# Kernel tuning notes

Measured on AMD Instinct MI355X. Metric: run time of the kernel, lower is better.

The kernel has to match this reference:

```python
import jax, jax.numpy as jnp
import numpy as np

B, S, D, H = 2, 4096, 1024, 16
HD = D // H  # 64


def setup_inputs() -> dict:
    key = jax.random.key(0)
    ks = jax.random.split(key, 6)
    return {
        "x": jax.random.normal(ks[0], (B, S, D), dtype=jnp.float32),
        "mask": jax.random.normal(ks[1], (B, S, S), dtype=jnp.float32),
        "Wqkv": jax.random.normal(ks[2], (D, 3 * D), dtype=jnp.float32) * 0.02,
        "bqkv": jax.random.normal(ks[3], (3 * D,), dtype=jnp.float32) * 0.02,
        "Wo": jax.random.normal(ks[4], (D, D), dtype=jnp.float32) * 0.02,
        "bo": jax.random.normal(ks[5], (D,), dtype=jnp.float32) * 0.02,
    }


def reference(x, mask, Wqkv, bqkv, Wo, bo):
    b, s, d = x.shape
    # fused QKV projection: [B,S,3D]
    qkv = jnp.einsum('bsd,de->bse', x, Wqkv) + bqkv
    # [B,S,H,3*HD] -> [B,H,S,3*HD]
    qkv = qkv.reshape(b, s, H, 3 * HD).transpose(0, 2, 1, 3)
    q, k, v = jnp.split(qkv, 3, axis=-1)  # each [B,H,S,HD]
    scale = 1.0 / jnp.sqrt(jnp.asarray(HD, dtype=x.dtype))
    scores = jnp.einsum('bhqe,bhke->bhqk', q, k) * scale  # [B,H,S,S]
    scores = scores + mask[:, None, :, :]  # additive mask broadcast over heads
    attn = jax.nn.softmax(scores, axis=-1)
    values = jnp.einsum('bhqk,bhke->bhqe', attn, v)  # [B,H,S,HD]
    # NOTE: faithful to original TF code: reshape WITHOUT transposing heads back
    values = values.reshape(b, s, d)
    out = jnp.einsum('bsd,de->bse', values, Wo) + bo
    return out
```

## Files before the change

kernel.cpp:

```cpp
#include <hip/hip_runtime.h>
#include <hip/hip_bf16.h>

#define DEV __device__ __forceinline__

typedef unsigned short u16;
typedef __attribute__((ext_vector_type(4))) float f32x4;
typedef __attribute__((ext_vector_type(8))) short s16x8;

static constexpr int Bc = 2, Hc = 16, Sc = 4096, Dc = 1024, HDc = 64;

DEV u16 f2bf(float f) {
  unsigned x = __float_as_uint(f);
  x += 0x7FFFu + ((x >> 16) & 1u);
  return (u16)(x >> 16);
}
DEV u16 f2bf_rn(float f) {
  return (u16)((__float_as_uint(f) + 0x8000u) >> 16);
}
DEV float bf2f(u16 u) { return __uint_as_float(((unsigned)u) << 16); }

DEV void gload_lds16(const void* g, void* l) {
  __builtin_amdgcn_global_load_lds((const __attribute__((address_space(1))) void*)g,
                                   (__attribute__((address_space(3))) void*)l, 16, 0, 0);
}

DEV f32x4 mfma16(s16x8 a, s16x8 b, f32x4 c) {
  return __builtin_amdgcn_mfma_f32_16x16x32_bf16(a, b, c, 0, 0, 0);
}

DEV f32x4 fzero4() { f32x4 v; v[0] = v[1] = v[2] = v[3] = 0.f; return v; }

__global__ void cvt_f32_bf16(const float* __restrict__ in, u16* __restrict__ out, size_t n,
                             float scale) {
  size_t i = ((size_t)blockIdx.x * blockDim.x + threadIdx.x) * 4;
  size_t stride = (size_t)gridDim.x * blockDim.x * 4;
  for (; i < n; i += stride) {
    float4 v = *(const float4*)(in + i);
    u16 a = f2bf(v.x * scale), b = f2bf(v.y * scale), c = f2bf(v.z * scale), d = f2bf(v.w * scale);
    *(ushort4*)(out + i) = make_ushort4(a, b, c, d);
  }
}

__global__ void transpose_cvt(const float* __restrict__ in, u16* __restrict__ out, int R, int C) {
  __shared__ u16 t[64][72];
  int nct = C >> 6;
  int tr = blockIdx.x / nct, tc = blockIdx.x % nct;
  int r0 = tr << 6, c0 = tc << 6;
  int lr = threadIdx.x >> 2;
  int lc0 = (threadIdx.x & 3) << 4;
  const float* src = in + (size_t)(r0 + lr) * C + c0 + lc0;
#pragma unroll
  for (int j = 0; j < 16; j += 4) {
    float4 v = *(const float4*)(src + j);
    t[lr][lc0 + j + 0] = f2bf(v.x);
    t[lr][lc0 + j + 1] = f2bf(v.y);
    t[lr][lc0 + j + 2] = f2bf(v.z);
    t[lr][lc0 + j + 3] = f2bf(v.w);
  }
  __syncthreads();
  u16* dst = out + (size_t)(c0 + lr) * R + r0 + lc0;
#pragma unroll
  for (int j = 0; j < 16; j += 4) {
    u16 a = t[lc0 + j + 0][lr], b = t[lc0 + j + 1][lr], c = t[lc0 + j + 2][lr], d = t[lc0 + j + 3][lr];
    *(ushort4*)(dst + j) = make_ushort4(a, b, c, d);
  }
}

template <int MODE>
__global__ __launch_bounds__(256, 2) void gemm128(
    const u16* __restrict__ A, const u16* __restrict__ BT, const float* __restrict__ bias,
    void* __restrict__ out0, u16* __restrict__ out1, u16* __restrict__ out2,
    int N, int K, int grid_n) {
  __shared__ u16 Al[128 * 64];
  __shared__ u16 Bl[128 * 64];
  int bid = blockIdx.x;
  int bn = bid % grid_n, bm = bid / grid_n;
  int m0 = bm * 128, n0 = bn * 128;
  int tid = threadIdx.x, lane = tid & 63, wid = tid >> 6;
  int wm = wid >> 1, wn = wid & 1;
  int fr = lane & 15, fg = lane >> 4;

  f32x4 acc[4][4];
#pragma unroll
  for (int mi = 0; mi < 4; ++mi)
#pragma unroll
    for (int ni = 0; ni < 4; ++ni) acc[mi][ni] = fzero4();

  for (int kt = 0; kt < K; kt += 64) {
    const u16* Ag = A + (size_t)m0 * K + kt;
    const u16* Bg = BT + (size_t)n0 * K + kt;
#pragma unroll
    for (int it = 0; it < 4; ++it) {
      int L = it * 4096 + wid * 1024 + lane * 16;
      int row = L >> 7;
      int sch = ((L >> 4) & 7) ^ (row & 7);
      gload_lds16(Ag + (size_t)row * K + sch * 8, (char*)Al + it * 4096 + wid * 1024);
      gload_lds16(Bg + (size_t)row * K + sch * 8, (char*)Bl + it * 4096 + wid * 1024);
    }
    __syncthreads();
#pragma unroll
    for (int c = 0; c < 2; ++c) {
      s16x8 af[4], bfr[4];
#pragma unroll
      for (int mi = 0; mi < 4; ++mi) {
        int row = wm * 64 + mi * 16 + fr;
        int ch = (c * 4 + fg) ^ (row & 7);
        af[mi] = *(const s16x8*)((const char*)Al + row * 128 + ch * 16);
      }
#pragma unroll
      for (int ni = 0; ni < 4; ++ni) {
        int row = wn * 64 + ni * 16 + fr;
        int ch = (c * 4 + fg) ^ (row & 7);
        bfr[ni] = *(const s16x8*)((const char*)Bl + row * 128 + ch * 16);
      }
#pragma unroll
      for (int mi = 0; mi < 4; ++mi)
#pragma unroll
        for (int ni = 0; ni < 4; ++ni) acc[mi][ni] = mfma16(af[mi], bfr[ni], acc[mi][ni]);
    }
    __syncthreads();
  }

  if constexpr (MODE == 0) {
    u16* qb = (u16*)out0;
    u16* kb = out1;
    u16* vT = out2;
#pragma unroll
    for (int ni = 0; ni < 4; ++ni) {
      int n = n0 + wn * 64 + ni * 16 + fr;
      float bv = bias[n];
      int h = n / 192;
      int c = n % 192;
      int part = c >> 6;
      int e = c & 63;
#pragma unroll
      for (int mi = 0; mi < 4; ++mi) {
        int m = m0 + wm * 64 + mi * 16 + fg * 4;
        int b = m >> 12;
        int s = m & 4095;
        size_t bh = (size_t)b * Hc + h;
        if (part == 2) {
          u16 a0 = f2bf(acc[mi][ni][0] + bv), a1 = f2bf(acc[mi][ni][1] + bv);
          u16 a2 = f2bf(acc[mi][ni][2] + bv), a3 = f2bf(acc[mi][ni][3] + bv);
          *(ushort4*)(vT + ((bh * HDc + e) * (size_t)Sc + s)) = make_ushort4(a0, a1, a2, a3);
        } else {
          u16* dst = (part == 0 ? qb : kb) + ((bh * Sc + s) * (size_t)HDc + e);
#pragma unroll
          for (int r = 0; r < 4; ++r) dst[(size_t)r * HDc] = f2bf(acc[mi][ni][r] + bv);
        }
      }
    }
  } else {
    float* O = (float*)out0;
#pragma unroll
    for (int ni = 0; ni < 4; ++ni) {
      int n = n0 + wn * 64 + ni * 16 + fr;
      float bv = bias[n];
#pragma unroll
      for (int mi = 0; mi < 4; ++mi) {
        int m = m0 + wm * 64 + mi * 16 + fg * 4;
#pragma unroll
        for (int r = 0; r < 4; ++r) O[(size_t)(m + r) * N + n] = acc[mi][ni][r] + bv;
      }
    }
  }
}

__global__ __launch_bounds__(256, 2) void attn_kernel(
    const u16* __restrict__ qb, const u16* __restrict__ kb, const u16* __restrict__ vT,
    const void* __restrict__ maskp, int mask_is_bf16, u16* __restrict__ vals) {
  __shared__ u16 Kl[64 * 64];
  __shared__ u16 Vl[64 * 64];
  __shared__ char Pl[4 * 16 * 144];
  int bid = blockIdx.x;
  int h = bid & 15, b = (bid >> 4) & 1, qt = bid >> 5;
  int lane = threadIdx.x & 63, wid = threadIdx.x >> 6;
  int fr = lane & 15, fg = lane >> 4;
  size_t bh = (size_t)b * Hc + h;
  int q0 = qt * 64;
  int q = q0 + wid * 16 + fr;

  const u16* Qrow = qb + ((bh * Sc) + q) * (size_t)HDc;
  s16x8 qa0 = *(const s16x8*)(Qrow + fg * 8);
  s16x8 qa1 = *(const s16x8*)(Qrow + 32 + fg * 8);

  f32x4 o[4];
#pragma unroll
  for (int ef = 0; ef < 4; ++ef) o[ef] = fzero4();
  float mrun = -1e30f, lrun = 0.f;

  const u16* Kg = kb + bh * (size_t)Sc * HDc;
  const u16* Vg = vT + bh * (size_t)HDc * Sc;
  char* pw = (char*)Pl + wid * 2304 + fr * 144;
  const float SCALE2 = 0.125f * 1.44269504088896340736f;
  const float LOG2E = 1.44269504088896340736f;

  int ch0 = (0 * 4 + fg) ^ (fr & 7);
  int ch1 = (1 * 4 + fg) ^ (fr & 7);

  const u16* mk_b = (const u16*)maskp + ((size_t)b * Sc + q) * Sc;
  const float* mk_f = (const float*)maskp + ((size_t)b * Sc + q) * Sc;

  for (int kt = 0; kt < Sc / 64; ++kt) {
#pragma unroll
    for (int it = 0; it < 2; ++it) {
      int L = it * 4096 + wid * 1024 + lane * 16;
      int row = L >> 7;
      int sch = ((L >> 4) & 7) ^ (row & 7);
      gload_lds16(Kg + ((size_t)(kt * 64 + row)) * HDc + sch * 8, (char*)Kl + it * 4096 + wid * 1024);
      gload_lds16(Vg + (size_t)row * Sc + kt * 64 + sch * 8, (char*)Vl + it * 4096 + wid * 1024);
    }
    __syncthreads();

    ushort4 m4[4];
    float4 mf[4];
    if (mask_is_bf16) {
#pragma unroll
      for (int f = 0; f < 4; ++f)
        m4[f] = *(const ushort4*)(mk_b + kt * 64 + f * 16 + fg * 4);
    } else {
#pragma unroll
      for (int f = 0; f < 4; ++f)
        mf[f] = *(const float4*)(mk_f + kt * 64 + f * 16 + fg * 4);
    }

    f32x4 sa[4];
#pragma unroll
    for (int f = 0; f < 4; ++f) sa[f] = fzero4();
#pragma unroll
    for (int c = 0; c < 2; ++c) {
      s16x8 qa = (c == 0) ? qa0 : qa1;
      int ch = (c == 0) ? ch0 : ch1;
#pragma unroll
      for (int f = 0; f < 4; ++f) {
        s16x8 kf = *(const s16x8*)((const char*)Kl + (f * 16 + fr) * 128 + ch * 16);
        sa[f] = mfma16(kf, qa, sa[f]);
      }
    }

    float sv[4][4];
    if (mask_is_bf16) {
#pragma unroll
      for (int f = 0; f < 4; ++f) {
        sv[f][0] = fmaf(sa[f][0], SCALE2, bf2f(m4[f].x));
        sv[f][1] = fmaf(sa[f][1], SCALE2, bf2f(m4[f].y));
        sv[f][2] = fmaf(sa[f][2], SCALE2, bf2f(m4[f].z));
        sv[f][3] = fmaf(sa[f][3], SCALE2, bf2f(m4[f].w));
      }
    } else {
#pragma unroll
      for (int f = 0; f < 4; ++f) {
        sv[f][0] = fmaf(sa[f][0], SCALE2, mf[f].x * LOG2E);
        sv[f][1] = fmaf(sa[f][1], SCALE2, mf[f].y * LOG2E);
        sv[f][2] = fmaf(sa[f][2], SCALE2, mf[f].z * LOG2E);
        sv[f][3] = fmaf(sa[f][3], SCALE2, mf[f].w * LOG2E);
      }
    }

    float mt = fmaxf(fmaxf(fmaxf(sv[0][0], sv[0][1]), fmaxf(sv[0][2], sv[0][3])),
                     fmaxf(fmaxf(sv[1][0], sv[1][1]), fmaxf(sv[1][2], sv[1][3])));
    float mt2 = fmaxf(fmaxf(fmaxf(sv[2][0], sv[2][1]), fmaxf(sv[2][2], sv[2][3])),
                      fmaxf(fmaxf(sv[3][0], sv[3][1]), fmaxf(sv[3][2], sv[3][3])));
    mt = fmaxf(mt, mt2);
    mt = fmaxf(mt, __shfl_xor(mt, 16, 64));
    mt = fmaxf(mt, __shfl_xor(mt, 32, 64));
    float mnew = fmaxf(mrun, mt);
    float alph = __builtin_amdgcn_exp2f(mrun - mnew);
    mrun = mnew;

    float p[4][4];
    float ssum = 0.f;
#pragma unroll
    for (int f = 0; f < 4; ++f) {
      float s0 = __builtin_amdgcn_exp2f(sv[f][0] - mnew);
      float s1 = __builtin_amdgcn_exp2f(sv[f][1] - mnew);
      float s2 = __builtin_amdgcn_exp2f(sv[f][2] - mnew);
      float s3 = __builtin_amdgcn_exp2f(sv[f][3] - mnew);
      p[f][0] = s0; p[f][1] = s1; p[f][2] = s2; p[f][3] = s3;
      ssum += (s0 + s1) + (s2 + s3);
    }
    ssum += __shfl_xor(ssum, 16, 64);
    ssum += __shfl_xor(ssum, 32, 64);
    lrun = fmaf(lrun, alph, ssum);

#pragma unroll
    for (int ef = 0; ef < 4; ++ef) o[ef] *= alph;

#pragma unroll
    for (int f = 0; f < 4; ++f) {
      ushort4 pk = make_ushort4(f2bf_rn(p[f][0]), f2bf_rn(p[f][1]),
                                f2bf_rn(p[f][2]), f2bf_rn(p[f][3]));
      *(ushort4*)(pw + f * 32 + fg * 8) = pk;
    }

#pragma unroll
    for (int c = 0; c < 2; ++c) {
      s16x8 pa = *(const s16x8*)(pw + c * 64 + fg * 16);
      int ch = (c == 0) ? ch0 : ch1;
#pragma unroll
      for (int ef = 0; ef < 4; ++ef) {
        s16x8 vf = *(const s16x8*)((const char*)Vl + (ef * 16 + fr) * 128 + ch * 16);
        o[ef] = mfma16(vf, pa, o[ef]);
      }
    }
    __syncthreads();
  }

  float inv = 1.f / lrun;
  u16* vbase = vals + (size_t)b * Sc * Dc + (size_t)h * Sc * HDc + (size_t)q * HDc;
#pragma unroll
  for (int ef = 0; ef < 4; ++ef) {
    ushort4 ov = make_ushort4(f2bf(o[ef][0] * inv), f2bf(o[ef][1] * inv),
                              f2bf(o[ef][2] * inv), f2bf(o[ef][3] * inv));
    *(ushort4*)(vbase + ef * 16 + fg * 4) = ov;
  }
}

extern "C" void kernel_launch(void* const* d_in, const int* in_sizes, int n_in,
                              void* d_out, int out_size, void* d_ws, size_t ws_size,
                              hipStream_t stream) {
  (void)in_sizes; (void)n_in; (void)out_size;
  const float* x    = (const float*)d_in[0];
  const float* mask = (const float*)d_in[1];
  const float* Wqkv = (const float*)d_in[2];
  const float* bqkv = (const float*)d_in[3];
  const float* Wo   = (const float*)d_in[4];
  const float* bo   = (const float*)d_in[5];
  float* out = (float*)d_out;
  char* ws = (char*)d_ws;

  u16* xb    = (u16*)(ws + 0);
  u16* wqkvT = (u16*)(ws + 16777216);
  u16* woT   = (u16*)(ws + 23068672);
  u16* qb    = (u16*)(ws + 25165824);
  u16* kb    = (u16*)(ws + 41943040);
  u16* vT    = (u16*)(ws + 58720256);
  u16* vals  = (u16*)(ws + 75497472);
  u16* maskb = (u16*)(ws + 92274688);
  int use_mb = (ws_size >= 159383552ull) ? 1 : 0;
  const float LOG2E = 1.44269504088896340736f;

  cvt_f32_bf16<<<dim3(2048), dim3(256), 0, stream>>>(x, xb, (size_t)8388608, 1.0f);
  if (use_mb)
    cvt_f32_bf16<<<dim3(4096), dim3(256), 0, stream>>>(mask, maskb, (size_t)33554432, LOG2E);
  transpose_cvt<<<dim3(768), dim3(256), 0, stream>>>(Wqkv, wqkvT, 1024, 3072);
  transpose_cvt<<<dim3(256), dim3(256), 0, stream>>>(Wo, woT, 1024, 1024);

  gemm128<0><<<dim3(1536), dim3(256), 0, stream>>>(xb, wqkvT, bqkv, (void*)qb, kb, vT,
                                                   3072, 1024, 24);
  attn_kernel<<<dim3(2048), dim3(256), 0, stream>>>(qb, kb, vT,
      use_mb ? (const void*)maskb : (const void*)mask, use_mb, vals);
  gemm128<1><<<dim3(512), dim3(256), 0, stream>>>(vals, woT, bo, (void*)out, nullptr, nullptr,
                                                  1024, 1024, 8);
}
```

Baseline: 464.6 us.

## Double-buffer K/V tiles, read fp32 mask directly, add lazy softmax rescaling

```diff
diff --git a/kernel.cpp b/kernel.cpp
--- a/kernel.cpp
+++ b/kernel.cpp
@@ -14,10 +14,13 @@
   x += 0x7FFFu + ((x >> 16) & 1u);
   return (u16)(x >> 16);
 }
-DEV u16 f2bf_rn(float f) {
-  return (u16)((__float_as_uint(f) + 0x8000u) >> 16);
-}
 DEV float bf2f(u16 u) { return __uint_as_float(((unsigned)u) << 16); }
+
+DEV unsigned cvtpk_bf16(float lo, float hi) {
+  unsigned r;
+  asm("v_cvt_pk_bf16_f32 %0, %1, %2" : "=v"(r) : "v"(lo), "v"(hi));
+  return r;
+}
 
 DEV void gload_lds16(const void* g, void* l) {
   __builtin_amdgcn_global_load_lds((const __attribute__((address_space(1))) void*)g,
@@ -30,13 +33,12 @@
 
 DEV f32x4 fzero4() { f32x4 v; v[0] = v[1] = v[2] = v[3] = 0.f; return v; }
 
-__global__ void cvt_f32_bf16(const float* __restrict__ in, u16* __restrict__ out, size_t n,
-                             float scale) {
+__global__ void cvt_f32_bf16(const float* __restrict__ in, u16* __restrict__ out, size_t n) {
   size_t i = ((size_t)blockIdx.x * blockDim.x + threadIdx.x) * 4;
   size_t stride = (size_t)gridDim.x * blockDim.x * 4;
   for (; i < n; i += stride) {
     float4 v = *(const float4*)(in + i);
-    u16 a = f2bf(v.x * scale), b = f2bf(v.y * scale), c = f2bf(v.z * scale), d = f2bf(v.w * scale);
+    u16 a = f2bf(v.x), b = f2bf(v.y), c = f2bf(v.z), d = f2bf(v.w);
     *(ushort4*)(out + i) = make_ushort4(a, b, c, d);
   }
 }
@@ -168,11 +170,12 @@
 
 __global__ __launch_bounds__(256, 2) void attn_kernel(
     const u16* __restrict__ qb, const u16* __restrict__ kb, const u16* __restrict__ vT,
-    const void* __restrict__ maskp, int mask_is_bf16, u16* __restrict__ vals) {
-  __shared__ u16 Kl[64 * 64];
-  __shared__ u16 Vl[64 * 64];
+    const float* __restrict__ maskp, u16* __restrict__ vals) {
+  __shared__ u16 Kl[2][64 * 64];
+  __shared__ u16 Vl[2][64 * 64];
   __shared__ char Pl[4 * 16 * 144];
-  int bid = blockIdx.x;
+
+  int bid = ((blockIdx.x & 7) << 8) | (blockIdx.x >> 3);
   int h = bid & 15, b = (bid >> 4) & 1, qt = bid >> 5;
   int lane = threadIdx.x & 63, wid = threadIdx.x >> 6;
   int fr = lane & 15, fg = lane >> 4;
@@ -192,117 +195,138 @@
   const u16* Kg = kb + bh * (size_t)Sc * HDc;
   const u16* Vg = vT + bh * (size_t)HDc * Sc;
   char* pw = (char*)Pl + wid * 2304 + fr * 144;
-  const float SCALE2 = 0.125f * 1.44269504088896340736f;
+  const float SCALE = 0.125f;
   const float LOG2E = 1.44269504088896340736f;
 
-  int ch0 = (0 * 4 + fg) ^ (fr & 7);
-  int ch1 = (1 * 4 + fg) ^ (fr & 7);
-
-  const u16* mk_b = (const u16*)maskp + ((size_t)b * Sc + q) * Sc;
-  const float* mk_f = (const float*)maskp + ((size_t)b * Sc + q) * Sc;
+  int L0 = wid * 1024 + lane * 16;
+  int L1 = 4096 + wid * 1024 + lane * 16;
+  int row0 = L0 >> 7, row1 = L1 >> 7;
+  int sch0s = ((L0 >> 4) & 7) ^ (row0 & 7);
+  int sch1s = ((L1 >> 4) & 7) ^ (row1 & 7);
+  const u16* KgS0 = Kg + (size_t)row0 * HDc + sch0s * 8;
+  const u16* KgS1 = Kg + (size_t)row1 * HDc + sch1s * 8;
+  const u16* VgS0 = Vg + (size_t)row0 * Sc + sch0s * 8;
+  const u16* VgS1 = Vg + (size_t)row1 * Sc + sch1s * 8;
+  int ldsA = wid * 1024;
+  int ldsB = 4096 + wid * 1024;
+
+  int ch0 = fg ^ (fr & 7);
+  int ch1 = (4 + fg) ^ (fr & 7);
+  int kroff0 = fr * 128 + ch0 * 16;
+  int kroff1 = fr * 128 + ch1 * 16;
+
+  const float* mk = maskp + ((size_t)b * Sc + q) * Sc;
+
+  gload_lds16(KgS0, (char*)Kl[0] + ldsA);
+  gload_lds16(KgS1, (char*)Kl[0] + ldsB);
+  gload_lds16(VgS0, (char*)Vl[0] + ldsA);
+  gload_lds16(VgS1, (char*)Vl[0] + ldsB);
+  __syncthreads();
 
   for (int kt = 0; kt < Sc / 64; ++kt) {
-#pragma unroll
-    for (int it = 0; it < 2; ++it) {
-      int L = it * 4096 + wid * 1024 + lane * 16;
-      int row = L >> 7;
-      int sch = ((L >> 4) & 7) ^ (row & 7);
-      gload_lds16(Kg + ((size_t)(kt * 64 + row)) * HDc + sch * 8, (char*)Kl + it * 4096 + wid * 1024);
-      gload_lds16(Vg + (size_t)row * Sc + kt * 64 + sch * 8, (char*)Vl + it * 4096 + wid * 1024);
-    }
-    __syncthreads();
-
-    ushort4 m4[4];
-    float4 mf[4];
-    if (mask_is_bf16) {
-#pragma unroll
-      for (int f = 0; f < 4; ++f)
-        m4[f] = *(const ushort4*)(mk_b + kt * 64 + f * 16 + fg * 4);
-    } else {
-#pragma unroll
-      for (int f = 0; f < 4; ++f)
-        mf[f] = *(const float4*)(mk_f + kt * 64 + f * 16 + fg * 4);
-    }
-
+    int cur = kt & 1;
+    if (kt < Sc / 64 - 1) {
+      int nxt = cur ^ 1;
+      size_t ko = (size_t)(kt + 1) * 64 * HDc;
+      size_t vo = (size_t)(kt + 1) * 64;
+      gload_lds16(KgS0 + ko, (char*)Kl[nxt] + ldsA);
+      gload_lds16(KgS1 + ko, (char*)Kl[nxt] + ldsB);
+      gload_lds16(VgS0 + vo, (char*)Vl[nxt] + ldsA);
+      gload_lds16(VgS1 + vo, (char*)Vl[nxt] + ldsB);
+    }
+
+    const float* mrow = mk + kt * 64 + fg * 4;
+    float4 mf0 = *(const float4*)(mrow);
+    float4 mf1 = *(const float4*)(mrow + 16);
+    float4 mf2 = *(const float4*)(mrow + 32);
+    float4 mf3 = *(const float4*)(mrow + 48);
+
+    const char* Kc = (const char*)Kl[cur];
     f32x4 sa[4];
 #pragma unroll
     for (int f = 0; f < 4; ++f) sa[f] = fzero4();
-#pragma unroll
-    for (int c = 0; c < 2; ++c) {
-      s16x8 qa = (c == 0) ? qa0 : qa1;
-      int ch = (c == 0) ? ch0 : ch1;
-#pragma unroll
-      for (int f = 0; f < 4; ++f) {
-        s16x8 kf = *(const s16x8*)((const char*)Kl + (f * 16 + fr) * 128 + ch * 16);
-        sa[f] = mfma16(kf, qa, sa[f]);
-      }
-    }
-
-    float sv[4][4];
-    if (mask_is_bf16) {
-#pragma unroll
-      for (int f = 0; f < 4; ++f) {
-        sv[f][0] = fmaf(sa[f][0], SCALE2, bf2f(m4[f].x));
-        sv[f][1] = fmaf(sa[f][1], SCALE2, bf2f(m4[f].y));
-        sv[f][2] = fmaf(sa[f][2], SCALE2, bf2f(m4[f].z));
-        sv[f][3] = fmaf(sa[f][3], SCALE2, bf2f(m4[f].w));
-      }
-    } else {
-#pragma unroll
-      for (int f = 0; f < 4; ++f) {
-        sv[f][0] = fmaf(sa[f][0], SCALE2, mf[f].x * LOG2E);
-        sv[f][1] = fmaf(sa[f][1], SCALE2, mf[f].y * LOG2E);
-        sv[f][2] = fmaf(sa[f][2], SCALE2, mf[f].z * LOG2E);
-        sv[f][3] = fmaf(sa[f][3], SCALE2, mf[f].w * LOG2E);
-      }
-    }
-
-    float mt = fmaxf(fmaxf(fmaxf(sv[0][0], sv[0][1]), fmaxf(sv[0][2], sv[0][3])),
-                     fmaxf(fmaxf(sv[1][0], sv[1][1]), fmaxf(sv[1][2], sv[1][3])));
-    float mt2 = fmaxf(fmaxf(fmaxf(sv[2][0], sv[2][1]), fmaxf(sv[2][2], sv[2][3])),
-                      fmaxf(fmaxf(sv[3][0], sv[3][1]), fmaxf(sv[3][2], sv[3][3])));
-    mt = fmaxf(mt, mt2);
+    __builtin_amdgcn_s_setprio(1);
+#pragma unroll
+    for (int f = 0; f < 4; ++f) {
+      s16x8 kf = *(const s16x8*)(Kc + f * 2048 + kroff0);
+      sa[f] = mfma16(kf, qa0, sa[f]);
+    }
+#pragma unroll
+    for (int f = 0; f < 4; ++f) {
+      s16x8 kf = *(const s16x8*)(Kc + f * 2048 + kroff1);
+      sa[f] = mfma16(kf, qa1, sa[f]);
+    }
+    __builtin_amdgcn_s_setprio(0);
+
+    float t[4][4];
+#pragma unroll
+    for (int r = 0; r < 4; ++r) {
+      t[0][r] = fmaf(sa[0][r], SCALE, (&mf0.x)[r]);
+      t[1][r] = fmaf(sa[1][r], SCALE, (&mf1.x)[r]);
+      t[2][r] = fmaf(sa[2][r], SCALE, (&mf2.x)[r]);
+      t[3][r] = fmaf(sa[3][r], SCALE, (&mf3.x)[r]);
+    }
+
+    float x0 = fmaxf(fmaxf(t[0][0], t[0][1]), t[0][2]);
+    float x1 = fmaxf(fmaxf(t[0][3], t[1][0]), t[1][1]);
+    float x2 = fmaxf(fmaxf(t[1][2], t[1][3]), t[2][0]);
+    float x3 = fmaxf(fmaxf(t[2][1], t[2][2]), t[2][3]);
+    float x4 = fmaxf(fmaxf(t[3][0], t[3][1]), t[3][2]);
+    float mt = fmaxf(fmaxf(fmaxf(x0, x1), x2), fmaxf(fmaxf(x3, x4), t[3][3]));
     mt = fmaxf(mt, __shfl_xor(mt, 16, 64));
     mt = fmaxf(mt, __shfl_xor(mt, 32, 64));
-    float mnew = fmaxf(mrun, mt);
-    float alph = __builtin_amdgcn_exp2f(mrun - mnew);
-    mrun = mnew;
-
+
+    if (!__all(mt <= mrun + 8.0f)) {
+      float mnew = fmaxf(mrun, mt);
+      float al = __builtin_amdgcn_exp2f((mrun - mnew) * LOG2E);
+      mrun = mnew;
+      lrun *= al;
+#pragma unroll
+      for (int ef = 0; ef < 4; ++ef) o[ef] *= al;
+    }
+
+    float nm = -mrun * LOG2E;
     float p[4][4];
-    float ssum = 0.f;
+    float ss0 = 0.f, ss1 = 0.f;
 #pragma unroll
     for (int f = 0; f < 4; ++f) {
-      float s0 = __builtin_amdgcn_exp2f(sv[f][0] - mnew);
-      float s1 = __builtin_amdgcn_exp2f(sv[f][1] - mnew);
-      float s2 = __builtin_amdgcn_exp2f(sv[f][2] - mnew);
-      float s3 = __builtin_amdgcn_exp2f(sv[f][3] - mnew);
-      p[f][0] = s0; p[f][1] = s1; p[f][2] = s2; p[f][3] = s3;
-      ssum += (s0 + s1) + (s2 + s3);
-    }
+      float p0 = __builtin_amdgcn_exp2f(fmaf(t[f][0], LOG2E, nm));
+      float p1 = __builtin_amdgcn_exp2f(fmaf(t[f][1], LOG2E, nm));
+      float p2 = __builtin_amdgcn_exp2f(fmaf(t[f][2], LOG2E, nm));
+      float p3 = __builtin_amdgcn_exp2f(fmaf(t[f][3], LOG2E, nm));
+      p[f][0] = p0; p[f][1] = p1; p[f][2] = p2; p[f][3] = p3;
+      ss0 += (p0 + p1);
+      ss1 += (p2 + p3);
+    }
+    float ssum = ss0 + ss1;
     ssum += __shfl_xor(ssum, 16, 64);
     ssum += __shfl_xor(ssum, 32, 64);
-    lrun = fmaf(lrun, alph, ssum);
-
-#pragma unroll
-    for (int ef = 0; ef < 4; ++ef) o[ef] *= alph;
+    lrun += ssum;
 
 #pragma unroll
     for (int f = 0; f < 4; ++f) {
-      ushort4 pk = make_ushort4(f2bf_rn(p[f][0]), f2bf_rn(p[f][1]),
-                                f2bf_rn(p[f][2]), f2bf_rn(p[f][3]));
-      *(ushort4*)(pw + f * 32 + fg * 8) = pk;
-    }
-
-#pragma unroll
-    for (int c = 0; c < 2; ++c) {
-      s16x8 pa = *(const s16x8*)(pw + c * 64 + fg * 16);
-      int ch = (c == 0) ? ch0 : ch1;
-#pragma unroll
-      for (int ef = 0; ef < 4; ++ef) {
-        s16x8 vf = *(const s16x8*)((const char*)Vl + (ef * 16 + fr) * 128 + ch * 16);
-        o[ef] = mfma16(vf, pa, o[ef]);
-      }
-    }
+      uint2 pk;
+      pk.x = cvtpk_bf16(p[f][0], p[f][1]);
+      pk.y = cvtpk_bf16(p[f][2], p[f][3]);
+      *(uint2*)(pw + f * 32 + fg * 8) = pk;
+    }
+
+    const char* Vc = (const char*)Vl[cur];
+    s16x8 pa0 = *(const s16x8*)(pw + fg * 16);
+    s16x8 pa1 = *(const s16x8*)(pw + 64 + fg * 16);
+    __builtin_amdgcn_s_setprio(1);
+#pragma unroll
+    for (int ef = 0; ef < 4; ++ef) {
+      s16x8 vf = *(const s16x8*)(Vc + ef * 2048 + kroff0);
+      o[ef] = mfma16(vf, pa0, o[ef]);
+    }
+#pragma unroll
+    for (int ef = 0; ef < 4; ++ef) {
+      s16x8 vf = *(const s16x8*)(Vc + ef * 2048 + kroff1);
+      o[ef] = mfma16(vf, pa1, o[ef]);
+    }
+    __builtin_amdgcn_s_setprio(0);
+
     __syncthreads();
   }
 
@@ -319,7 +343,7 @@
 extern "C" void kernel_launch(void* const* d_in, const int* in_sizes, int n_in,
                               void* d_out, int out_size, void* d_ws, size_t ws_size,
                               hipStream_t stream) {
-  (void)in_sizes; (void)n_in; (void)out_size;
+  (void)in_sizes; (void)n_in; (void)out_size; (void)ws_size;
   const float* x    = (const float*)d_in[0];
   const float* mask = (const float*)d_in[1];
   const float* Wqkv = (const float*)d_in[2];
@@ -336,20 +360,14 @@
   u16* kb    = (u16*)(ws + 41943040);
   u16* vT    = (u16*)(ws + 58720256);
   u16* vals  = (u16*)(ws + 75497472);
-  u16* maskb = (u16*)(ws + 92274688);
-  int use_mb = (ws_size >= 159383552ull) ? 1 : 0;
-  const float LOG2E = 1.44269504088896340736f;
-
-  cvt_f32_bf16<<<dim3(2048), dim3(256), 0, stream>>>(x, xb, (size_t)8388608, 1.0f);
-  if (use_mb)
-    cvt_f32_bf16<<<dim3(4096), dim3(256), 0, stream>>>(mask, maskb, (size_t)33554432, LOG2E);
+
+  cvt_f32_bf16<<<dim3(2048), dim3(256), 0, stream>>>(x, xb, (size_t)8388608);
   transpose_cvt<<<dim3(768), dim3(256), 0, stream>>>(Wqkv, wqkvT, 1024, 3072);
   transpose_cvt<<<dim3(256), dim3(256), 0, stream>>>(Wo, woT, 1024, 1024);
 
   gemm128<0><<<dim3(1536), dim3(256), 0, stream>>>(xb, wqkvT, bqkv, (void*)qb, kb, vT,
                                                    3072, 1024, 24);
-  attn_kernel<<<dim3(2048), dim3(256), 0, stream>>>(qb, kb, vT,
-      use_mb ? (const void*)maskb : (const void*)mask, use_mb, vals);
+  attn_kernel<<<dim3(2048), dim3(256), 0, stream>>>(qb, kb, vT, mask, vals);
   gemm128<1><<<dim3(512), dim3(256), 0, stream>>>(vals, woT, bo, (void*)out, nullptr, nullptr,
                                                   1024, 1024, 8);
 }
```

Measured after the change: 451.7 us. 1.03x faster.
